# Kernel tuning notes

Hardware: AMD Instinct MI355X
Metric: run time of the kernel (lower is better)

The kernel has to match this reference:

```python
import jax, jax.numpy as jnp
import numpy as np

BATCH = 32768
D = 1024          # vector dimension
BITS = 4          # total bit budget
MSE_BITS = BITS - 1
K = 2 ** MSE_BITS # 8 codebook centroids
QJL_DIM = D       # default qjl projection dim


def setup_inputs() -> dict:
    key = jax.random.key(0)
    kx, kq, ks = jax.random.split(key, 3)
    x = jax.random.normal(kx, (BATCH, D), dtype=jnp.float32)
    # Haar-random rotation: QR of Gaussian with sign-fixed R diagonal
    G = jax.random.normal(kq, (D, D), dtype=jnp.float32)
    Q, R = jnp.linalg.qr(G)
    s = jnp.sign(jnp.diag(R))
    s = jnp.where(s == 0, 1.0, s)
    Pi = Q * s[None, :]
    # QJL projection matrix S: iid N(0,1), shape (m, d)
    S = jax.random.normal(ks, (QJL_DIM, D), dtype=jnp.float32)
    # Lloyd-Max-style scalar codebook for N(0,1): Gaussian quantile centroids
    probs = (jnp.arange(K, dtype=jnp.float32) + 0.5) / K
    centroids = (jnp.sqrt(2.0) * jax.scipy.special.erfinv(2.0 * probs - 1.0)).astype(jnp.float32)
    return {"x": x, "Pi": Pi, "centroids": centroids, "S": S}


def reference(x, Pi, centroids, S):
    # Stage 1 (MSE quantizer): rotate, per-coordinate nearest-centroid, gather, unrotate
    y = x @ Pi.T                                   # (B, D)
    diffs = jnp.abs(y[..., None] - centroids)      # (B, D, K)
    mse_indices = jnp.argmin(diffs, axis=-1)       # (B, D) int
    y_hat = centroids[mse_indices]                 # (B, D)
    x_hat = y_hat @ Pi                             # (B, D)
    # Stage 2 (QJL on residual)
    residual = x - x_hat                           # (B, D)
    residual_norm = jnp.linalg.norm(residual, axis=-1)  # (B,)
    projected = residual @ S.T                     # (B, m)
    qjl_signs = jnp.sign(projected)
    qjl_signs = jnp.where(qjl_signs == 0, 1.0, qjl_signs)
    return mse_indices, qjl_signs, residual_norm
```

## Files before the change

kernel.cpp:

```cpp
#include <hip/hip_runtime.h>
#include <math.h>

#define B_ROWS 32768
#define DIM    1024
#define PAD    140
#define LDSF   (2*2*32*PAD)


struct FragT { float4 a0, a1, a2, a3, b0, b1, b2, b3; };

__device__ __forceinline__ void loadT(const float* pA, const float* pB, FragT& f) {
    f.a0 = *(const float4*)(pA);
    f.a1 = *(const float4*)(pA + (size_t)32 * DIM);
    f.a2 = *(const float4*)(pA + (size_t)64 * DIM);
    f.a3 = *(const float4*)(pA + (size_t)96 * DIM);
    f.b0 = *(const float4*)(pB);
    f.b1 = *(const float4*)(pB + (size_t)32 * DIM);
    f.b2 = *(const float4*)(pB + (size_t)64 * DIM);
    f.b3 = *(const float4*)(pB + (size_t)96 * DIM);
}

__device__ __forceinline__ void storeT(const FragT& f, float (*As)[PAD], float (*Bs)[PAD],
                                       int kq, int r0) {
    const int c0 = kq * 4;
    const int sh = 4 * (kq >> 1);
#pragma unroll
    for (int i = 0; i < 4; ++i) {
        const float4 v = (i == 0) ? f.a0 : (i == 1) ? f.a1 : (i == 2) ? f.a2 : f.a3;
        const int col = r0 + 32 * i + sh;
        As[c0 + 0][col] = v.x; As[c0 + 1][col] = v.y;
        As[c0 + 2][col] = v.z; As[c0 + 3][col] = v.w;
    }
#pragma unroll
    for (int i = 0; i < 4; ++i) {
        const float4 v = (i == 0) ? f.b0 : (i == 1) ? f.b1 : (i == 2) ? f.b2 : f.b3;
        const int col = r0 + 32 * i + sh;
        Bs[c0 + 0][col] = v.x; Bs[c0 + 1][col] = v.y;
        Bs[c0 + 2][col] = v.z; Bs[c0 + 3][col] = v.w;
    }
}

__device__ __forceinline__ void computeT(const float (*As)[PAD], const float (*Bs)[PAD],
                                         int tx, int ty, float (&acc)[8][8]) {
#pragma unroll
    for (int kk = 0; kk < 32; ++kk) {
        const int sh = 4 * (kk >> 3);
        const float4 a0 = *(const float4*)&As[kk][ty * 8 + sh];
        const float4 a1 = *(const float4*)&As[kk][ty * 8 + 4 + sh];
        const float4 b0 = *(const float4*)&Bs[kk][tx * 4 + sh];
        const float4 b1 = *(const float4*)&Bs[kk][tx * 4 + 64 + sh];
        const float a[8] = {a0.x, a0.y, a0.z, a0.w, a1.x, a1.y, a1.z, a1.w};
        const float b[8] = {b0.x, b0.y, b0.z, b0.w, b1.x, b1.y, b1.z, b1.w};
#pragma unroll
        for (int i = 0; i < 8; ++i)
#pragma unroll
            for (int j = 0; j < 8; ++j)
                acc[i][j] = fmaf(a[i], b[j], acc[i][j]);
    }
}

__global__ __launch_bounds__(512) void k1_rot_quant(
    const float* __restrict__ X, const float* __restrict__ Pi, const float* __restrict__ C,
    float* __restrict__ idxf, unsigned char* __restrict__ idx8)
{
    __shared__ float lds[LDSF];
    const int tid = threadIdx.x, pan = tid >> 8, pt = tid & 255;
    float (*As)[PAD] = (float(*)[PAD])(lds + pan * 32 * PAD);
    float (*Bs)[PAD] = (float(*)[PAD])(lds + 2 * 32 * PAD + pan * 32 * PAD);
    const int tx = pt & 15, ty = pt >> 4;
    const int kq = pt & 7, r0 = pt >> 3;
    const int m0 = blockIdx.y * 128, n0 = blockIdx.x * 128;
    const float* pA = X  + (size_t)(m0 + r0) * DIM + pan * 512 + kq * 4;
    const float* pB = Pi + (size_t)(n0 + r0) * DIM + pan * 512 + kq * 4;
    float acc[8][8] = {};
    FragT f;
    loadT(pA, pB, f);
    for (int t = 0; t < 16; ++t) {
        __syncthreads();
        storeT(f, As, Bs, kq, r0);
        __syncthreads();
        if (t < 15) loadT(pA + (t + 1) * 32, pB + (t + 1) * 32, f);
        computeT(As, Bs, tx, ty, acc);
    }
    __syncthreads();
    if (pan == 1) {
#pragma unroll
        for (int i = 0; i < 8; ++i)
#pragma unroll
            for (int j = 0; j < 8; ++j)
                lds[(i * 8 + j) * 256 + pt] = acc[i][j];
    }
    __syncthreads();
    if (pan == 0) {
        float c8[8];
#pragma unroll
        for (int t = 0; t < 8; ++t) c8[t] = C[t];
#pragma unroll
        for (int i = 0; i < 8; ++i) {
            const size_t o = (size_t)(m0 + ty * 8 + i) * DIM + n0 + tx * 4;
            float fv[8]; unsigned char bv[8];
#pragma unroll
            for (int j = 0; j < 8; ++j) {
                const float y = acc[i][j] + lds[(i * 8 + j) * 256 + pt];
                float best = fabsf(y - c8[0]); int bi = 0;
#pragma unroll
                for (int t2 = 1; t2 < 8; ++t2) {
                    const float d = fabsf(y - c8[t2]);
                    if (d < best) { best = d; bi = t2; }
                }
                fv[j] = (float)bi; bv[j] = (unsigned char)bi;
            }
            *(float4*)&idxf[o]      = make_float4(fv[0], fv[1], fv[2], fv[3]);
            *(float4*)&idxf[o + 64] = make_float4(fv[4], fv[5], fv[6], fv[7]);
            *(uchar4*)&idx8[o]      = make_uchar4(bv[0], bv[1], bv[2], bv[3]);
            *(uchar4*)&idx8[o + 64] = make_uchar4(bv[4], bv[5], bv[6], bv[7]);
        }
    }
}

__global__ __launch_bounds__(512) void k3_unrot_residual(
    const float* __restrict__ X, const float* __restrict__ Pi, const float* __restrict__ C,
    const unsigned char* __restrict__ idx8, float* __restrict__ R, double* __restrict__ nrm2)
{
    __shared__ float lds[LDSF];
    __shared__ float clut[8];
    const int tid = threadIdx.x, pan = tid >> 8, pt = tid & 255;
    float (*As)[PAD] = (float(*)[PAD])(lds + pan * 32 * PAD);
    float (*Bs)[PAD] = (float(*)[PAD])(lds + 2 * 32 * PAD + pan * 32 * PAD);
    const int tx = pt & 15, ty = pt >> 4;
    const int kq = pt & 7, r0 = pt >> 3;
    const int nq = pt & 31, kr0 = pt >> 5;
    const int m0 = blockIdx.y * 128, n0 = blockIdx.x * 128;
    if (tid < 8) clut[tid] = C[tid];
    const unsigned char* pA = idx8 + (size_t)(m0 + r0) * DIM + pan * 512 + kq * 4;
    const float*         pB = Pi + (size_t)(pan * 512 + kr0) * DIM + n0 + nq * 4;
    float acc[8][8] = {};
    uchar4 ka[4]; float4 kb[4];
#pragma unroll
    for (int i = 0; i < 4; ++i) ka[i] = *(const uchar4*)(pA + (size_t)(32 * i) * DIM);
#pragma unroll
    for (int i = 0; i < 4; ++i) kb[i] = *(const float4*)(pB + (size_t)(8 * i) * DIM);
    for (int t = 0; t < 16; ++t) {
        __syncthreads();
        {
            const int c0 = kq * 4;
            const int sh = 4 * (kq >> 1);
#pragma unroll
            for (int i = 0; i < 4; ++i) {
                const int col = r0 + 32 * i + sh;
                As[c0 + 0][col] = clut[ka[i].x]; As[c0 + 1][col] = clut[ka[i].y];
                As[c0 + 2][col] = clut[ka[i].z]; As[c0 + 3][col] = clut[ka[i].w];
            }
#pragma unroll
            for (int i = 0; i < 4; ++i)
                *(float4*)&Bs[kr0 + 8 * i][nq * 4 + 4 * i] = kb[i];
        }
        __syncthreads();
        if (t < 15) {
#pragma unroll
            for (int i = 0; i < 4; ++i)
                ka[i] = *(const uchar4*)(pA + (t + 1) * 32 + (size_t)(32 * i) * DIM);
#pragma unroll
            for (int i = 0; i < 4; ++i)
                kb[i] = *(const float4*)(pB + (size_t)((t + 1) * 32 + 8 * i) * DIM);
        }
        computeT(As, Bs, tx, ty, acc);
    }
    __syncthreads();
    if (pan == 1) {
#pragma unroll
        for (int i = 0; i < 8; ++i)
#pragma unroll
            for (int j = 0; j < 8; ++j)
                lds[(i * 8 + j) * 256 + pt] = acc[i][j];
    }
    __syncthreads();
    if (pan == 0) {
#pragma unroll
        for (int i = 0; i < 8; ++i) {
            const int row = m0 + ty * 8 + i;
            const size_t o = (size_t)row * DIM + n0 + tx * 4;
            const float4 x0 = *(const float4*)&X[o];
            const float4 x1 = *(const float4*)&X[o + 64];
            float rv[8];
            rv[0] = x0.x - (acc[i][0] + lds[(i * 8 + 0) * 256 + pt]);
            rv[1] = x0.y - (acc[i][1] + lds[(i * 8 + 1) * 256 + pt]);
            rv[2] = x0.z - (acc[i][2] + lds[(i * 8 + 2) * 256 + pt]);
            rv[3] = x0.w - (acc[i][3] + lds[(i * 8 + 3) * 256 + pt]);
            rv[4] = x1.x - (acc[i][4] + lds[(i * 8 + 4) * 256 + pt]);
            rv[5] = x1.y - (acc[i][5] + lds[(i * 8 + 5) * 256 + pt]);
            rv[6] = x1.z - (acc[i][6] + lds[(i * 8 + 6) * 256 + pt]);
            rv[7] = x1.w - (acc[i][7] + lds[(i * 8 + 7) * 256 + pt]);
            *(float4*)&R[o]      = make_float4(rv[0], rv[1], rv[2], rv[3]);
            *(float4*)&R[o + 64] = make_float4(rv[4], rv[5], rv[6], rv[7]);
            double s = 0.0;
#pragma unroll
            for (int j = 0; j < 8; ++j) s = fma((double)rv[j], (double)rv[j], s);
#pragma unroll
            for (int mask = 1; mask < 16; mask <<= 1) s += __shfl_xor(s, mask, 16);
            if (tx == 0) atomicAdd(&nrm2[row], s);
        }
    }
}

__global__ __launch_bounds__(512) void k5_qjl(
    const float* __restrict__ R, const float* __restrict__ S, float* __restrict__ sgn)
{
    __shared__ float lds[LDSF];
    const int tid = threadIdx.x, pan = tid >> 8, pt = tid & 255;
    float (*As)[PAD] = (float(*)[PAD])(lds + pan * 32 * PAD);
    float (*Bs)[PAD] = (float(*)[PAD])(lds + 2 * 32 * PAD + pan * 32 * PAD);
    const int tx = pt & 15, ty = pt >> 4;
    const int kq = pt & 7, r0 = pt >> 3;
    const int m0 = blockIdx.y * 128, n0 = blockIdx.x * 128;
    const float* pA = R + (size_t)(m0 + r0) * DIM + pan * 512 + kq * 4;
    const float* pB = S + (size_t)(n0 + r0) * DIM + pan * 512 + kq * 4;
    float acc[8][8] = {};
    FragT f;
    loadT(pA, pB, f);
    for (int t = 0; t < 16; ++t) {
        __syncthreads();
        storeT(f, As, Bs, kq, r0);
        __syncthreads();
        if (t < 15) loadT(pA + (t + 1) * 32, pB + (t + 1) * 32, f);
        computeT(As, Bs, tx, ty, acc);
    }
    __syncthreads();
    if (pan == 1) {
#pragma unroll
        for (int i = 0; i < 8; ++i)
#pragma unroll
            for (int j = 0; j < 8; ++j)
                lds[(i * 8 + j) * 256 + pt] = acc[i][j];
    }
    __syncthreads();
    if (pan == 0) {
#pragma unroll
        for (int i = 0; i < 8; ++i) {
            const size_t o = (size_t)(m0 + ty * 8 + i) * DIM + n0 + tx * 4;
            float pv[8];
#pragma unroll
            for (int j = 0; j < 8; ++j) pv[j] = acc[i][j] + lds[(i * 8 + j) * 256 + pt];
            *(float4*)&sgn[o]      = make_float4((pv[0] >= 0.f) ? 1.f : -1.f, (pv[1] >= 0.f) ? 1.f : -1.f,
                                                 (pv[2] >= 0.f) ? 1.f : -1.f, (pv[3] >= 0.f) ? 1.f : -1.f);
            *(float4*)&sgn[o + 64] = make_float4((pv[4] >= 0.f) ? 1.f : -1.f, (pv[5] >= 0.f) ? 1.f : -1.f,
                                                 (pv[6] >= 0.f) ? 1.f : -1.f, (pv[7] >= 0.f) ? 1.f : -1.f);
        }
    }
}

__global__ __launch_bounds__(256) void kN_sqrt(const double* __restrict__ nrm2, float* __restrict__ nrm)
{
    const int i = blockIdx.x * 256 + threadIdx.x;
    if (i < B_ROWS) nrm[i] = (float)sqrt(nrm2[i]);
}

extern "C" void kernel_launch(void* const* d_in, const int* in_sizes, int n_in,
                              void* d_out, int out_size, void* d_ws, size_t ws_size,
                              hipStream_t stream) {
    const float* X  = (const float*)d_in[0];
    const float* Pi = (const float*)d_in[1];
    const float* C  = (const float*)d_in[2];
    const float* S  = (const float*)d_in[3];

    float* out  = (float*)d_out;
    float* idxf = out;
    float* sgn  = out + (size_t)B_ROWS * DIM;
    float* nrm  = sgn + (size_t)B_ROWS * DIM;

    char* ws = (char*)d_ws;
    float*         R    = (float*)ws;
    unsigned char* idx8 = (unsigned char*)(ws + (size_t)B_ROWS * DIM * 4);
    double*        nrm2 = (double*)(ws + (size_t)B_ROWS * DIM * 5);

    hipMemsetAsync(nrm2, 0, (size_t)B_ROWS * sizeof(double), stream);

    dim3 blk(512);
    dim3 gG(DIM / 128, B_ROWS / 128);

    k1_rot_quant     <<<gG, blk, 0, stream>>>(X, Pi, C, idxf, idx8);
    k3_unrot_residual<<<gG, blk, 0, stream>>>(X, Pi, C, idx8, R, nrm2);
    kN_sqrt          <<<dim3(B_ROWS / 256), dim3(256), 0, stream>>>(nrm2, nrm);
    k5_qjl           <<<gG, blk, 0, stream>>>(R, S, sgn);
}
```

Measured before the change: 2.728 ms.

## Split-K GEMMs into separate kernels with larger 256x128 per-block tiles

Each of the three GEMMs is now split into two K-halves run as separate kernels. The first kernel writes partial sums into the sign output buffer, and the second adds them and applies the epilogue. This replaces the intra-block two-panel split-K with LDS reduction, and grows each thread's tile from 8x8 to 16x8 with 256-thread blocks, raising FMA work per LDS load. In exchange it adds global round-trips for the partial sums, launches more kernels, and raises register pressure from the 128 accumulators per thread.

```diff
diff --git a/kernel.cpp b/kernel.cpp
--- a/kernel.cpp
+++ b/kernel.cpp
@@ -3,76 +3,65 @@
 
 #define B_ROWS 32768
 #define DIM    1024
-#define PAD    140
-#define LDSF   (2*2*32*PAD)
-
-
-struct FragT { float4 a0, a1, a2, a3, b0, b1, b2, b3; };
+#define PADA   268
+#define PADB   140
+
+
+struct FragT { float4 a[8]; float4 b[4]; };
 
 __device__ __forceinline__ void loadT(const float* pA, const float* pB, FragT& f) {
-    f.a0 = *(const float4*)(pA);
-    f.a1 = *(const float4*)(pA + (size_t)32 * DIM);
-    f.a2 = *(const float4*)(pA + (size_t)64 * DIM);
-    f.a3 = *(const float4*)(pA + (size_t)96 * DIM);
-    f.b0 = *(const float4*)(pB);
-    f.b1 = *(const float4*)(pB + (size_t)32 * DIM);
-    f.b2 = *(const float4*)(pB + (size_t)64 * DIM);
-    f.b3 = *(const float4*)(pB + (size_t)96 * DIM);
-}
-
-__device__ __forceinline__ void storeT(const FragT& f, float (*As)[PAD], float (*Bs)[PAD],
+#pragma unroll
+    for (int i = 0; i < 8; ++i) f.a[i] = *(const float4*)(pA + (size_t)(32 * i) * DIM);
+#pragma unroll
+    for (int i = 0; i < 4; ++i) f.b[i] = *(const float4*)(pB + (size_t)(32 * i) * DIM);
+}
+
+__device__ __forceinline__ void storeT(const FragT& f, float (*As)[PADA], float (*Bs)[PADB],
                                        int kq, int r0) {
-    const int c0 = kq * 4;
-    const int sh = 4 * (kq >> 1);
+    const int c0 = kq * 4, sh = 4 * (kq >> 1);
+#pragma unroll
+    for (int i = 0; i < 8; ++i) {
+        const int col = r0 + 32 * i + sh;
+        As[c0 + 0][col] = f.a[i].x; As[c0 + 1][col] = f.a[i].y;
+        As[c0 + 2][col] = f.a[i].z; As[c0 + 3][col] = f.a[i].w;
+    }
 #pragma unroll
     for (int i = 0; i < 4; ++i) {
-        const float4 v = (i == 0) ? f.a0 : (i == 1) ? f.a1 : (i == 2) ? f.a2 : f.a3;
         const int col = r0 + 32 * i + sh;
-        As[c0 + 0][col] = v.x; As[c0 + 1][col] = v.y;
-        As[c0 + 2][col] = v.z; As[c0 + 3][col] = v.w;
-    }
-#pragma unroll
-    for (int i = 0; i < 4; ++i) {
-        const float4 v = (i == 0) ? f.b0 : (i == 1) ? f.b1 : (i == 2) ? f.b2 : f.b3;
-        const int col = r0 + 32 * i + sh;
-        Bs[c0 + 0][col] = v.x; Bs[c0 + 1][col] = v.y;
-        Bs[c0 + 2][col] = v.z; Bs[c0 + 3][col] = v.w;
-    }
-}
-
-__device__ __forceinline__ void computeT(const float (*As)[PAD], const float (*Bs)[PAD],
-                                         int tx, int ty, float (&acc)[8][8]) {
+        Bs[c0 + 0][col] = f.b[i].x; Bs[c0 + 1][col] = f.b[i].y;
+        Bs[c0 + 2][col] = f.b[i].z; Bs[c0 + 3][col] = f.b[i].w;
+    }
+}
+
+__device__ __forceinline__ void compute16x8(const float (*As)[PADA], const float (*Bs)[PADB],
+                                            int tx, int ty, float (&acc)[16][8]) {
 #pragma unroll
     for (int kk = 0; kk < 32; ++kk) {
         const int sh = 4 * (kk >> 3);
-        const float4 a0 = *(const float4*)&As[kk][ty * 8 + sh];
-        const float4 a1 = *(const float4*)&As[kk][ty * 8 + 4 + sh];
-        const float4 b0 = *(const float4*)&Bs[kk][tx * 4 + sh];
-        const float4 b1 = *(const float4*)&Bs[kk][tx * 4 + 64 + sh];
-        const float a[8] = {a0.x, a0.y, a0.z, a0.w, a1.x, a1.y, a1.z, a1.w};
-        const float b[8] = {b0.x, b0.y, b0.z, b0.w, b1.x, b1.y, b1.z, b1.w};
-#pragma unroll
-        for (int i = 0; i < 8; ++i)
+        const float4 A0 = *(const float4*)&As[kk][4 * ty + sh];
+        const float4 A1 = *(const float4*)&As[kk][4 * ty + 64 + sh];
+        const float4 A2 = *(const float4*)&As[kk][4 * ty + 128 + sh];
+        const float4 A3 = *(const float4*)&As[kk][4 * ty + 192 + sh];
+        const float4 B0 = *(const float4*)&Bs[kk][4 * tx + sh];
+        const float4 B1 = *(const float4*)&Bs[kk][4 * tx + 64 + sh];
+        const float a[16] = {A0.x, A0.y, A0.z, A0.w, A1.x, A1.y, A1.z, A1.w,
+                             A2.x, A2.y, A2.z, A2.w, A3.x, A3.y, A3.z, A3.w};
+        const float b[8]  = {B0.x, B0.y, B0.z, B0.w, B1.x, B1.y, B1.z, B1.w};
+#pragma unroll
+        for (int i = 0; i < 16; ++i)
 #pragma unroll
             for (int j = 0; j < 8; ++j)
                 acc[i][j] = fmaf(a[i], b[j], acc[i][j]);
     }
 }
 
-__global__ __launch_bounds__(512) void k1_rot_quant(
-    const float* __restrict__ X, const float* __restrict__ Pi, const float* __restrict__ C,
-    float* __restrict__ idxf, unsigned char* __restrict__ idx8)
-{
-    __shared__ float lds[LDSF];
-    const int tid = threadIdx.x, pan = tid >> 8, pt = tid & 255;
-    float (*As)[PAD] = (float(*)[PAD])(lds + pan * 32 * PAD);
-    float (*Bs)[PAD] = (float(*)[PAD])(lds + 2 * 32 * PAD + pan * 32 * PAD);
-    const int tx = pt & 15, ty = pt >> 4;
-    const int kq = pt & 7, r0 = pt >> 3;
-    const int m0 = blockIdx.y * 128, n0 = blockIdx.x * 128;
-    const float* pA = X  + (size_t)(m0 + r0) * DIM + pan * 512 + kq * 4;
-    const float* pB = Pi + (size_t)(n0 + r0) * DIM + pan * 512 + kq * 4;
-    float acc[8][8] = {};
+__device__ __forceinline__ void runT(const float* Ab, const float* Bb, int m0, int n0,
+                                     int koff, int tid,
+                                     float (*As)[PADA], float (*Bs)[PADB],
+                                     float (&acc)[16][8]) {
+    const int tx = tid & 15, ty = tid >> 4, kq = tid & 7, r0 = tid >> 3;
+    const float* pA = Ab + (size_t)(m0 + r0) * DIM + koff + kq * 4;
+    const float* pB = Bb + (size_t)(n0 + r0) * DIM + koff + kq * 4;
     FragT f;
     loadT(pA, pB, f);
     for (int t = 0; t < 16; ++t) {
@@ -80,73 +69,29 @@
         storeT(f, As, Bs, kq, r0);
         __syncthreads();
         if (t < 15) loadT(pA + (t + 1) * 32, pB + (t + 1) * 32, f);
-        computeT(As, Bs, tx, ty, acc);
-    }
-    __syncthreads();
-    if (pan == 1) {
-#pragma unroll
-        for (int i = 0; i < 8; ++i)
-#pragma unroll
-            for (int j = 0; j < 8; ++j)
-                lds[(i * 8 + j) * 256 + pt] = acc[i][j];
-    }
-    __syncthreads();
-    if (pan == 0) {
-        float c8[8];
-#pragma unroll
-        for (int t = 0; t < 8; ++t) c8[t] = C[t];
-#pragma unroll
-        for (int i = 0; i < 8; ++i) {
-            const size_t o = (size_t)(m0 + ty * 8 + i) * DIM + n0 + tx * 4;
-            float fv[8]; unsigned char bv[8];
-#pragma unroll
-            for (int j = 0; j < 8; ++j) {
-                const float y = acc[i][j] + lds[(i * 8 + j) * 256 + pt];
-                float best = fabsf(y - c8[0]); int bi = 0;
-#pragma unroll
-                for (int t2 = 1; t2 < 8; ++t2) {
-                    const float d = fabsf(y - c8[t2]);
-                    if (d < best) { best = d; bi = t2; }
-                }
-                fv[j] = (float)bi; bv[j] = (unsigned char)bi;
-            }
-            *(float4*)&idxf[o]      = make_float4(fv[0], fv[1], fv[2], fv[3]);
-            *(float4*)&idxf[o + 64] = make_float4(fv[4], fv[5], fv[6], fv[7]);
-            *(uchar4*)&idx8[o]      = make_uchar4(bv[0], bv[1], bv[2], bv[3]);
-            *(uchar4*)&idx8[o + 64] = make_uchar4(bv[4], bv[5], bv[6], bv[7]);
-        }
-    }
-}
-
-__global__ __launch_bounds__(512) void k3_unrot_residual(
-    const float* __restrict__ X, const float* __restrict__ Pi, const float* __restrict__ C,
-    const unsigned char* __restrict__ idx8, float* __restrict__ R, double* __restrict__ nrm2)
-{
-    __shared__ float lds[LDSF];
-    __shared__ float clut[8];
-    const int tid = threadIdx.x, pan = tid >> 8, pt = tid & 255;
-    float (*As)[PAD] = (float(*)[PAD])(lds + pan * 32 * PAD);
-    float (*Bs)[PAD] = (float(*)[PAD])(lds + 2 * 32 * PAD + pan * 32 * PAD);
-    const int tx = pt & 15, ty = pt >> 4;
-    const int kq = pt & 7, r0 = pt >> 3;
-    const int nq = pt & 31, kr0 = pt >> 5;
-    const int m0 = blockIdx.y * 128, n0 = blockIdx.x * 128;
-    if (tid < 8) clut[tid] = C[tid];
-    const unsigned char* pA = idx8 + (size_t)(m0 + r0) * DIM + pan * 512 + kq * 4;
-    const float*         pB = Pi + (size_t)(pan * 512 + kr0) * DIM + n0 + nq * 4;
-    float acc[8][8] = {};
-    uchar4 ka[4]; float4 kb[4];
-#pragma unroll
-    for (int i = 0; i < 4; ++i) ka[i] = *(const uchar4*)(pA + (size_t)(32 * i) * DIM);
+        compute16x8(As, Bs, tx, ty, acc);
+    }
+}
+
+__device__ __forceinline__ void runG(const unsigned char* idxb, const float* Pi,
+                                     const float* clut, int m0, int n0, int koff, int tid,
+                                     float (*As)[PADA], float (*Bs)[PADB],
+                                     float (&acc)[16][8]) {
+    const int tx = tid & 15, ty = tid >> 4, kq = tid & 7, r0 = tid >> 3;
+    const int nq = tid & 31, kr0 = tid >> 5;
+    const unsigned char* pA = idxb + (size_t)(m0 + r0) * DIM + koff + kq * 4;
+    const float*         pB = Pi + (size_t)(koff + kr0) * DIM + n0 + nq * 4;
+    uchar4 ka[8]; float4 kb[4];
+#pragma unroll
+    for (int i = 0; i < 8; ++i) ka[i] = *(const uchar4*)(pA + (size_t)(32 * i) * DIM);
 #pragma unroll
     for (int i = 0; i < 4; ++i) kb[i] = *(const float4*)(pB + (size_t)(8 * i) * DIM);
     for (int t = 0; t < 16; ++t) {
         __syncthreads();
         {
-            const int c0 = kq * 4;
-            const int sh = 4 * (kq >> 1);
-#pragma unroll
-            for (int i = 0; i < 4; ++i) {
+            const int c0 = kq * 4, sh = 4 * (kq >> 1);
+#pragma unroll
+            for (int i = 0; i < 8; ++i) {
                 const int col = r0 + 32 * i + sh;
                 As[c0 + 0][col] = clut[ka[i].x]; As[c0 + 1][col] = clut[ka[i].y];
                 As[c0 + 2][col] = clut[ka[i].z]; As[c0 + 3][col] = clut[ka[i].w];
@@ -158,94 +103,152 @@
         __syncthreads();
         if (t < 15) {
 #pragma unroll
-            for (int i = 0; i < 4; ++i)
+            for (int i = 0; i < 8; ++i)
                 ka[i] = *(const uchar4*)(pA + (t + 1) * 32 + (size_t)(32 * i) * DIM);
 #pragma unroll
             for (int i = 0; i < 4; ++i)
                 kb[i] = *(const float4*)(pB + (size_t)((t + 1) * 32 + 8 * i) * DIM);
         }
-        computeT(As, Bs, tx, ty, acc);
-    }
-    __syncthreads();
-    if (pan == 1) {
-#pragma unroll
-        for (int i = 0; i < 8; ++i)
-#pragma unroll
-            for (int j = 0; j < 8; ++j)
-                lds[(i * 8 + j) * 256 + pt] = acc[i][j];
-    }
-    __syncthreads();
-    if (pan == 0) {
-#pragma unroll
-        for (int i = 0; i < 8; ++i) {
-            const int row = m0 + ty * 8 + i;
-            const size_t o = (size_t)row * DIM + n0 + tx * 4;
-            const float4 x0 = *(const float4*)&X[o];
-            const float4 x1 = *(const float4*)&X[o + 64];
-            float rv[8];
-            rv[0] = x0.x - (acc[i][0] + lds[(i * 8 + 0) * 256 + pt]);
-            rv[1] = x0.y - (acc[i][1] + lds[(i * 8 + 1) * 256 + pt]);
-            rv[2] = x0.z - (acc[i][2] + lds[(i * 8 + 2) * 256 + pt]);
-            rv[3] = x0.w - (acc[i][3] + lds[(i * 8 + 3) * 256 + pt]);
-            rv[4] = x1.x - (acc[i][4] + lds[(i * 8 + 4) * 256 + pt]);
-            rv[5] = x1.y - (acc[i][5] + lds[(i * 8 + 5) * 256 + pt]);
-            rv[6] = x1.z - (acc[i][6] + lds[(i * 8 + 6) * 256 + pt]);
-            rv[7] = x1.w - (acc[i][7] + lds[(i * 8 + 7) * 256 + pt]);
-            *(float4*)&R[o]      = make_float4(rv[0], rv[1], rv[2], rv[3]);
-            *(float4*)&R[o + 64] = make_float4(rv[4], rv[5], rv[6], rv[7]);
-            double s = 0.0;
-#pragma unroll
-            for (int j = 0; j < 8; ++j) s = fma((double)rv[j], (double)rv[j], s);
-#pragma unroll
-            for (int mask = 1; mask < 16; mask <<= 1) s += __shfl_xor(s, mask, 16);
-            if (tx == 0) atomicAdd(&nrm2[row], s);
+        compute16x8(As, Bs, tx, ty, acc);
+    }
+}
+
+__global__ __launch_bounds__(256) void kT_part(
+    const float* __restrict__ A, const float* __restrict__ B, float* __restrict__ part)
+{
+    __shared__ float As[32][PADA];
+    __shared__ float Bs[32][PADB];
+    const int tid = threadIdx.x, tx = tid & 15, ty = tid >> 4;
+    const int m0 = blockIdx.y * 256, n0 = blockIdx.x * 128;
+    float acc[16][8] = {};
+    runT(A, B, m0, n0, 0, tid, As, Bs, acc);
+#pragma unroll
+    for (int i = 0; i < 16; ++i) {
+        const int row = m0 + 64 * (i >> 2) + 4 * ty + (i & 3);
+        const size_t o = (size_t)row * DIM + n0 + tx * 4;
+        *(float4*)&part[o]      = make_float4(acc[i][0], acc[i][1], acc[i][2], acc[i][3]);
+        *(float4*)&part[o + 64] = make_float4(acc[i][4], acc[i][5], acc[i][6], acc[i][7]);
+    }
+}
+
+__global__ __launch_bounds__(256) void k1_final(
+    const float* __restrict__ X, const float* __restrict__ Pi, const float* __restrict__ C,
+    const float* __restrict__ part, float* __restrict__ idxf, unsigned char* __restrict__ idx8)
+{
+    __shared__ float As[32][PADA];
+    __shared__ float Bs[32][PADB];
+    const int tid = threadIdx.x, tx = tid & 15, ty = tid >> 4;
+    const int m0 = blockIdx.y * 256, n0 = blockIdx.x * 128;
+    float acc[16][8] = {};
+    runT(X, Pi, m0, n0, 512, tid, As, Bs, acc);
+    float c8[8];
+#pragma unroll
+    for (int t = 0; t < 8; ++t) c8[t] = C[t];
+#pragma unroll
+    for (int i = 0; i < 16; ++i) {
+        const int row = m0 + 64 * (i >> 2) + 4 * ty + (i & 3);
+        const size_t o = (size_t)row * DIM + n0 + tx * 4;
+        const float4 p1l = *(const float4*)&part[o];
+        const float4 p1h = *(const float4*)&part[o + 64];
+        const float y[8] = {p1l.x + acc[i][0], p1l.y + acc[i][1], p1l.z + acc[i][2], p1l.w + acc[i][3],
+                            p1h.x + acc[i][4], p1h.y + acc[i][5], p1h.z + acc[i][6], p1h.w + acc[i][7]};
+        float fv[8]; unsigned char bv[8];
+#pragma unroll
+        for (int j = 0; j < 8; ++j) {
+            float best = fabsf(y[j] - c8[0]); int bi = 0;
+#pragma unroll
+            for (int t2 = 1; t2 < 8; ++t2) {
+                const float d = fabsf(y[j] - c8[t2]);
+                if (d < best) { best = d; bi = t2; }
+            }
+            fv[j] = (float)bi; bv[j] = (unsigned char)bi;
         }
-    }
-}
-
-__global__ __launch_bounds__(512) void k5_qjl(
-    const float* __restrict__ R, const float* __restrict__ S, float* __restrict__ sgn)
-{
-    __shared__ float lds[LDSF];
-    const int tid = threadIdx.x, pan = tid >> 8, pt = tid & 255;
-    float (*As)[PAD] = (float(*)[PAD])(lds + pan * 32 * PAD);
-    float (*Bs)[PAD] = (float(*)[PAD])(lds + 2 * 32 * PAD + pan * 32 * PAD);
-    const int tx = pt & 15, ty = pt >> 4;
-    const int kq = pt & 7, r0 = pt >> 3;
-    const int m0 = blockIdx.y * 128, n0 = blockIdx.x * 128;
-    const float* pA = R + (size_t)(m0 + r0) * DIM + pan * 512 + kq * 4;
-    const float* pB = S + (size_t)(n0 + r0) * DIM + pan * 512 + kq * 4;
-    float acc[8][8] = {};
-    FragT f;
-    loadT(pA, pB, f);
-    for (int t = 0; t < 16; ++t) {
-        __syncthreads();
-        storeT(f, As, Bs, kq, r0);
-        __syncthreads();
-        if (t < 15) loadT(pA + (t + 1) * 32, pB + (t + 1) * 32, f);
-        computeT(As, Bs, tx, ty, acc);
-    }
-    __syncthreads();
-    if (pan == 1) {
-#pragma unroll
-        for (int i = 0; i < 8; ++i)
-#pragma unroll
-            for (int j = 0; j < 8; ++j)
-                lds[(i * 8 + j) * 256 + pt] = acc[i][j];
-    }
-    __syncthreads();
-    if (pan == 0) {
-#pragma unroll
-        for (int i = 0; i < 8; ++i) {
-            const size_t o = (size_t)(m0 + ty * 8 + i) * DIM + n0 + tx * 4;
-            float pv[8];
-#pragma unroll
-            for (int j = 0; j < 8; ++j) pv[j] = acc[i][j] + lds[(i * 8 + j) * 256 + pt];
-            *(float4*)&sgn[o]      = make_float4((pv[0] >= 0.f) ? 1.f : -1.f, (pv[1] >= 0.f) ? 1.f : -1.f,
-                                                 (pv[2] >= 0.f) ? 1.f : -1.f, (pv[3] >= 0.f) ? 1.f : -1.f);
-            *(float4*)&sgn[o + 64] = make_float4((pv[4] >= 0.f) ? 1.f : -1.f, (pv[5] >= 0.f) ? 1.f : -1.f,
-                                                 (pv[6] >= 0.f) ? 1.f : -1.f, (pv[7] >= 0.f) ? 1.f : -1.f);
-        }
+        *(float4*)&idxf[o]      = make_float4(fv[0], fv[1], fv[2], fv[3]);
+        *(float4*)&idxf[o + 64] = make_float4(fv[4], fv[5], fv[6], fv[7]);
+        *(uchar4*)&idx8[o]      = make_uchar4(bv[0], bv[1], bv[2], bv[3]);
+        *(uchar4*)&idx8[o + 64] = make_uchar4(bv[4], bv[5], bv[6], bv[7]);
+    }
+}
+
+__global__ __launch_bounds__(256) void k3_part(
+    const unsigned char* __restrict__ idx8, const float* __restrict__ Pi,
+    const float* __restrict__ C, float* __restrict__ part)
+{
+    __shared__ float As[32][PADA];
+    __shared__ float Bs[32][PADB];
+    __shared__ float clut[8];
+    const int tid = threadIdx.x, tx = tid & 15, ty = tid >> 4;
+    const int m0 = blockIdx.y * 256, n0 = blockIdx.x * 128;
+    if (tid < 8) clut[tid] = C[tid];
+    float acc[16][8] = {};
+    runG(idx8, Pi, clut, m0, n0, 0, tid, As, Bs, acc);
+#pragma unroll
+    for (int i = 0; i < 16; ++i) {
+        const int row = m0 + 64 * (i >> 2) + 4 * ty + (i & 3);
+        const size_t o = (size_t)row * DIM + n0 + tx * 4;
+        *(float4*)&part[o]      = make_float4(acc[i][0], acc[i][1], acc[i][2], acc[i][3]);
+        *(float4*)&part[o + 64] = make_float4(acc[i][4], acc[i][5], acc[i][6], acc[i][7]);
+    }
+}
+
+__global__ __launch_bounds__(256) void k3_final(
+    const float* __restrict__ X, const float* __restrict__ Pi, const float* __restrict__ C,
+    const unsigned char* __restrict__ idx8, const float* __restrict__ part,
+    float* __restrict__ R, double* __restrict__ nrm2)
+{
+    __shared__ float As[32][PADA];
+    __shared__ float Bs[32][PADB];
+    __shared__ float clut[8];
+    const int tid = threadIdx.x, tx = tid & 15, ty = tid >> 4;
+    const int m0 = blockIdx.y * 256, n0 = blockIdx.x * 128;
+    if (tid < 8) clut[tid] = C[tid];
+    float acc[16][8] = {};
+    runG(idx8, Pi, clut, m0, n0, 512, tid, As, Bs, acc);
+#pragma unroll
+    for (int i = 0; i < 16; ++i) {
+        const int row = m0 + 64 * (i >> 2) + 4 * ty + (i & 3);
+        const size_t o = (size_t)row * DIM + n0 + tx * 4;
+        const float4 p1l = *(const float4*)&part[o];
+        const float4 p1h = *(const float4*)&part[o + 64];
+        const float4 x0 = *(const float4*)&X[o];
+        const float4 x1 = *(const float4*)&X[o + 64];
+        float rv[8];
+        rv[0] = x0.x - (p1l.x + acc[i][0]); rv[1] = x0.y - (p1l.y + acc[i][1]);
+        rv[2] = x0.z - (p1l.z + acc[i][2]); rv[3] = x0.w - (p1l.w + acc[i][3]);
+        rv[4] = x1.x - (p1h.x + acc[i][4]); rv[5] = x1.y - (p1h.y + acc[i][5]);
+        rv[6] = x1.z - (p1h.z + acc[i][6]); rv[7] = x1.w - (p1h.w + acc[i][7]);
+        *(float4*)&R[o]      = make_float4(rv[0], rv[1], rv[2], rv[3]);
+        *(float4*)&R[o + 64] = make_float4(rv[4], rv[5], rv[6], rv[7]);
+        double s = 0.0;
+#pragma unroll
+        for (int j = 0; j < 8; ++j) s = fma((double)rv[j], (double)rv[j], s);
+#pragma unroll
+        for (int mask = 1; mask < 16; mask <<= 1) s += __shfl_xor(s, mask, 16);
+        if (tx == 0) atomicAdd(&nrm2[row], s);
+    }
+}
+
+__global__ __launch_bounds__(256) void k5_final(
+    const float* __restrict__ R, const float* __restrict__ S, float* psgn)
+{
+    __shared__ float As[32][PADA];
+    __shared__ float Bs[32][PADB];
+    const int tid = threadIdx.x, tx = tid & 15, ty = tid >> 4;
+    const int m0 = blockIdx.y * 256, n0 = blockIdx.x * 128;
+    float acc[16][8] = {};
+    runT(R, S, m0, n0, 512, tid, As, Bs, acc);
+#pragma unroll
+    for (int i = 0; i < 16; ++i) {
+        const int row = m0 + 64 * (i >> 2) + 4 * ty + (i & 3);
+        const size_t o = (size_t)row * DIM + n0 + tx * 4;
+        const float4 p1l = *(const float4*)&psgn[o];
+        const float4 p1h = *(const float4*)&psgn[o + 64];
+        const float p[8] = {p1l.x + acc[i][0], p1l.y + acc[i][1], p1l.z + acc[i][2], p1l.w + acc[i][3],
+                            p1h.x + acc[i][4], p1h.y + acc[i][5], p1h.z + acc[i][6], p1h.w + acc[i][7]};
+        *(float4*)&psgn[o]      = make_float4((p[0] >= 0.f) ? 1.f : -1.f, (p[1] >= 0.f) ? 1.f : -1.f,
+                                              (p[2] >= 0.f) ? 1.f : -1.f, (p[3] >= 0.f) ? 1.f : -1.f);
+        *(float4*)&psgn[o + 64] = make_float4((p[4] >= 0.f) ? 1.f : -1.f, (p[5] >= 0.f) ? 1.f : -1.f,
+                                              (p[6] >= 0.f) ? 1.f : -1.f, (p[7] >= 0.f) ? 1.f : -1.f);
     }
 }
 
@@ -275,11 +278,14 @@
 
     hipMemsetAsync(nrm2, 0, (size_t)B_ROWS * sizeof(double), stream);
 
-    dim3 blk(512);
-    dim3 gG(DIM / 128, B_ROWS / 128);
-
-    k1_rot_quant     <<<gG, blk, 0, stream>>>(X, Pi, C, idxf, idx8);
-    k3_unrot_residual<<<gG, blk, 0, stream>>>(X, Pi, C, idx8, R, nrm2);
-    kN_sqrt          <<<dim3(B_ROWS / 256), dim3(256), 0, stream>>>(nrm2, nrm);
-    k5_qjl           <<<gG, blk, 0, stream>>>(R, S, sgn);
-}
+    dim3 blk(256);
+    dim3 gG(DIM / 128, B_ROWS / 256);
+
+    kT_part <<<gG, blk, 0, stream>>>(X, Pi, sgn);
+    k1_final<<<gG, blk, 0, stream>>>(X, Pi, C, sgn, idxf, idx8);
+    k3_part <<<gG, blk, 0, stream>>>(idx8, Pi, C, sgn);
+    k3_final<<<gG, blk, 0, stream>>>(X, Pi, C, idx8, sgn, R, nrm2);
+    kN_sqrt <<<dim3(B_ROWS / 256), blk, 0, stream>>>(nrm2, nrm);
+    kT_part <<<gG, blk, 0, stream>>>(R, S, sgn);
+    k5_final<<<gG, blk, 0, stream>>>(R, S, sgn);
+}
```

After: 2.852 ms. 1.05x slower.
